# Kernel optimization log

Hardware: AMD Instinct MI355X
Metric: run time of the kernel (lower is better)

Reference implementation:

```python
import jax, jax.numpy as jnp
import numpy as np

B, S, D, H = 2, 2048, 1024, 16
HEAD_DIM = D // H
SCALE = HEAD_DIM ** -0.5


def setup_inputs() -> dict:
    key = jax.random.key(0)
    k1, k2, k3 = jax.random.split(key, 3)
    x = jax.random.normal(k1, (B, S, D), dtype=jnp.float32)
    # torch nn.Linear convention: weight is [out_features, in_features], y = x @ W.T + b
    W_qkv = jax.random.normal(k2, (3 * D, D), dtype=jnp.float32) * 0.02  # qkv Linear, bias=False
    W_out = jax.random.normal(k3, (D, D), dtype=jnp.float32) * 0.02
    b_out = jnp.zeros((D,), dtype=jnp.float32)
    return {"x": x, "W_qkv": W_qkv, "W_out": W_out, "b_out": b_out}


def reference(x, W_qkv, W_out, b_out):
    b, s, d_model = x.shape
    # qkv projection (no bias), then split 'b c (qkv h d) -> qkv b h c d'
    qkv = (x @ W_qkv.T).reshape(b, s, 3, H, HEAD_DIM).transpose(2, 0, 3, 1, 4)
    q, k, v = qkv[0], qkv[1], qkv[2]  # each [b, h, s, hd]
    # naive full attention: scores materialized as [b, h, s, s]
    attn = jax.nn.softmax(jnp.einsum('bhxd,bhyd->bhxy', q, k) * SCALE, axis=-1)
    # dropout is identity (rate 0 / eval mode)
    o = jnp.einsum('bhxy,bhyd->bhxd', attn, v)
    o = o.transpose(0, 2, 1, 3).reshape(b, s, d_model)  # 'b h c d -> b c (h d)'
    return o @ W_out.T + b_out
```

## Files before the change

### kernel.cpp

```cpp
#include <hip/hip_runtime.h>


typedef __attribute__((ext_vector_type(8))) short short8;
typedef __attribute__((ext_vector_type(4))) float f32x4;
typedef unsigned short ushort_t;
typedef unsigned int uint32;

#define AS1 __attribute__((address_space(1)))
#define AS3 __attribute__((address_space(3)))

__device__ __forceinline__ void gload_lds16(const void* gp, void* lp) {
    __builtin_amdgcn_global_load_lds((const AS1 void*)gp, (AS3 void*)lp, 16, 0, 0);
}

#if __has_builtin(__builtin_amdgcn_exp2f)
#define EXP2F(x) __builtin_amdgcn_exp2f(x)
#else
#define EXP2F(x) exp2f(x)
#endif

__device__ __forceinline__ uint32 rhu(float f) { return __float_as_uint(f) + 0x8000u; }
#if __has_builtin(__builtin_amdgcn_perm)
__device__ __forceinline__ uint32 pk2bf(float a, float b) {
    return __builtin_amdgcn_perm(rhu(b), rhu(a), 0x07060302u);
}
#else
__device__ __forceinline__ uint32 pk2bf(float a, float b) {
    return (rhu(a) >> 16) | (rhu(b) & 0xffff0000u);
}
#endif
__device__ __forceinline__ ushort_t f2bf(float f) { return (ushort_t)(rhu(f) >> 16); }

__global__ void cvt_all(const float* __restrict__ x, ushort_t* __restrict__ xb,
                        const float* __restrict__ wq, ushort_t* __restrict__ wqb,
                        const float* __restrict__ wo, ushort_t* __restrict__ wob) {
    int blk = blockIdx.x;
    const float* in; ushort_t* out;
    if (blk < 4096)      { in = x;  out = xb;  }
    else if (blk < 7168) { in = wq; out = wqb; blk -= 4096; }
    else                 { in = wo; out = wob; blk -= 7168; }
    const int i = (blk * 256 + threadIdx.x) * 4;
    const float4 v = *(const float4*)(in + i);
    uint2 pk;
    pk.x = pk2bf(v.x, v.y);
    pk.y = pk2bf(v.z, v.w);
    *(uint2*)(out + i) = pk;
}

__global__ __launch_bounds__(256, 2)
void gemm_bt_bf16(const ushort_t* __restrict__ A, const ushort_t* __restrict__ B,
                  ushort_t* __restrict__ Cb, float* __restrict__ Cf,
                  const float* __restrict__ bias, ushort_t* __restrict__ vT,
                  int M, int N, int K, int ldc, float qScale) {
    __shared__ ushort_t lA[128 * 32];
    __shared__ ushort_t lB[128 * 32];
    const int tid = threadIdx.x;
    const int wave = tid >> 6, lane = tid & 63;
    const int quad = lane >> 4, l16 = lane & 15;
    const int wr = wave >> 1, wc = wave & 1;
    const int mBase = blockIdx.y * 128, nBase = blockIdx.x * 128;

    f32x4 acc[4][4];
#pragma unroll
    for (int i = 0; i < 4; i++)
#pragma unroll
        for (int j = 0; j < 4; j++) acc[i][j] = (f32x4){0.f, 0.f, 0.f, 0.f};

    const int ar = tid >> 2;
    const int ac = (((tid & 3) ^ ((ar >> 1) & 3)) * 8);
    const int rsw = ((l16 >> 1) & 3);

    const ushort_t* aptr = A + (size_t)(mBase + ar) * K + ac;
    const ushort_t* bptr = B + (size_t)(nBase + ar) * K + ac;

    for (int k0 = 0; k0 < K; k0 += 32) {
#pragma unroll
        for (int c = 0; c < 2; c++) {
            gload_lds16(aptr + (size_t)(c * 64) * K + k0, lA + c * 2048 + wave * 512);
            gload_lds16(bptr + (size_t)(c * 64) * K + k0, lB + c * 2048 + wave * 512);
        }
        __syncthreads();

        short8 af[4], bf[4];
#pragma unroll
        for (int i = 0; i < 4; i++)
            af[i] = *(const short8*)(lA + (wr * 64 + i * 16 + l16) * 32 + ((quad ^ rsw) * 8));
#pragma unroll
        for (int j = 0; j < 4; j++)
            bf[j] = *(const short8*)(lB + (wc * 64 + j * 16 + l16) * 32 + ((quad ^ rsw) * 8));
#pragma unroll
        for (int i = 0; i < 4; i++)
#pragma unroll
            for (int j = 0; j < 4; j++)
                acc[i][j] = __builtin_amdgcn_mfma_f32_16x16x32_bf16(af[i], bf[j], acc[i][j], 0, 0, 0);
        __syncthreads();
    }

    if (vT && nBase >= 2048) {
#pragma unroll
        for (int i = 0; i < 4; i++)
#pragma unroll
            for (int j = 0; j < 4; j++) {
                const int row0 = mBase + wr * 64 + i * 16 + quad * 4;
                const int col = nBase + wc * 64 + j * 16 + l16 - 2048;
                const int b = row0 >> 11, s0 = row0 & 2047;
                uint2 pk;
                pk.x = pk2bf(acc[i][j][0], acc[i][j][1]);
                pk.y = pk2bf(acc[i][j][2], acc[i][j][3]);
                *(uint2*)(vT + ((size_t)(b * 16) * 64 + col) * 2048 + s0) = pk;
            }
        return;
    }
    const float cs = (vT && nBase < 1024) ? qScale : 1.0f;
#pragma unroll
    for (int i = 0; i < 4; i++)
#pragma unroll
        for (int j = 0; j < 4; j++)
#pragma unroll
            for (int r = 0; r < 4; r++) {
                const int row = mBase + wr * 64 + i * 16 + quad * 4 + r;
                const int col = nBase + wc * 64 + j * 16 + l16;
                const float v = acc[i][j][r];
                if (Cb) Cb[(size_t)row * ldc + col] = f2bf(v * cs);
                else    Cf[(size_t)row * ldc + col] = v + bias[col];
            }
}

__global__ __launch_bounds__(256, 4)
void attn_flash(const ushort_t* __restrict__ qk, const ushort_t* __restrict__ vT,
                ushort_t* __restrict__ o) {
    __shared__ ushort_t lK[128 * 64];
    __shared__ ushort_t lV[64 * 128];
    __shared__ ushort_t lP[4][16 * 40];

    const int tid = threadIdx.x;
    const int wave = tid >> 6, lane = tid & 63;
    const int quad = lane >> 4, l16 = lane & 15;
    const int bh = blockIdx.y;
    const int b = bh >> 4, h = bh & 15;
    const size_t rowBase = (size_t)b * 2048;
    const int qCol = h * 64, kCol = 1024 + h * 64;
    const int qRow0 = blockIdx.x * 64;
    const int swz = (l16 & 7);

    const int sr = tid >> 3;
    const int sc = ((tid & 7) ^ (sr & 7)) * 8;
    const int vr = tid >> 4;
    const int vc = ((tid & 15) ^ (vr & 7)) * 8;

#pragma unroll
    for (int cc = 0; cc < 2; cc++)
        gload_lds16(qk + (rowBase + qRow0 + cc * 32 + sr) * 2048 + qCol + sc,
                    lK + cc * 2048 + wave * 512);
    __syncthreads();
    short8 qf[2];
#pragma unroll
    for (int ks = 0; ks < 2; ks++)
        qf[ks] = *(const short8*)(lK + (wave * 16 + l16) * 64 + (((ks * 4 + quad) ^ swz) * 8));
    __syncthreads();

    short8 onesA;
#pragma unroll
    for (int i = 0; i < 8; i++) onesA[i] = (short)0x3F80;

    f32x4 oacc[4];
    f32x4 lacc = (f32x4){0.f, 0.f, 0.f, 0.f};
#pragma unroll
    for (int dt = 0; dt < 4; dt++) oacc[dt] = (f32x4){0.f, 0.f, 0.f, 0.f};

    const ushort_t* kptr = qk + (rowBase + sr) * 2048 + kCol + sc;
    const ushort_t* vptr = vT + ((size_t)bh * 64 + vr) * 2048 + vc;

    for (int kt = 0; kt < 16; kt++) {
#pragma unroll
        for (int cc = 0; cc < 4; cc++)
            gload_lds16(kptr + (size_t)(cc * 32) * 2048, lK + cc * 2048 + wave * 512);
#pragma unroll
        for (int cc = 0; cc < 4; cc++)
            gload_lds16(vptr + (size_t)(cc * 16) * 2048, lV + cc * 2048 + wave * 512);
        kptr += 128 * 2048;
        vptr += 128;
        __syncthreads();

        f32x4 sacc[8];
#pragma unroll
        for (int mt = 0; mt < 8; mt++) {
            const short8 k0 = *(const short8*)(lK + (mt * 16 + l16) * 64 + ((quad ^ swz) * 8));
            const short8 k1 = *(const short8*)(lK + (mt * 16 + l16) * 64 + (((4 + quad) ^ swz) * 8));
            f32x4 t = (f32x4){0.f, 0.f, 0.f, 0.f};
            t = __builtin_amdgcn_mfma_f32_16x16x32_bf16(k0, qf[0], t, 0, 0, 0);
            t = __builtin_amdgcn_mfma_f32_16x16x32_bf16(k1, qf[1], t, 0, 0, 0);
            sacc[mt] = t;
        }

#pragma unroll
        for (int kk = 0; kk < 4; kk++) {
#pragma unroll
            for (int t16 = 0; t16 < 2; t16++) {
                const f32x4 s = sacc[2 * kk + t16];
                uint2 pk;
                pk.x = pk2bf(EXP2F(s[0]), EXP2F(s[1]));
                pk.y = pk2bf(EXP2F(s[2]), EXP2F(s[3]));
                *(uint2*)(&lP[wave][l16 * 40 + t16 * 16 + quad * 4]) = pk;
            }
            const short8 pf = *(const short8*)(&lP[wave][l16 * 40 + quad * 8]);
            lacc = __builtin_amdgcn_mfma_f32_16x16x32_bf16(onesA, pf, lacc, 0, 0, 0);
#pragma unroll
            for (int dt = 0; dt < 4; dt++) {
                const short8 vf = *(const short8*)(lV + (dt * 16 + l16) * 128 +
                                                   (((kk * 4 + quad) ^ swz) * 8));
                oacc[dt] = __builtin_amdgcn_mfma_f32_16x16x32_bf16(vf, pf, oacc[dt], 0, 0, 0);
            }
        }
        __syncthreads();
    }

    const float inv = 1.0f / lacc[0];
    const size_t row = rowBase + qRow0 + wave * 16 + l16;
#pragma unroll
    for (int dt = 0; dt < 4; dt++) {
        uint2 pk;
        pk.x = pk2bf(oacc[dt][0] * inv, oacc[dt][1] * inv);
        pk.y = pk2bf(oacc[dt][2] * inv, oacc[dt][3] * inv);
        *(uint2*)(o + row * 1024 + h * 64 + dt * 16 + quad * 4) = pk;
    }
}

extern "C" void kernel_launch(void* const* d_in, const int* in_sizes, int n_in,
                              void* d_out, int out_size, void* d_ws, size_t ws_size,
                              hipStream_t stream) {
    const float* x    = (const float*)d_in[0];
    const float* Wqkv = (const float*)d_in[1];
    const float* Wout = (const float*)d_in[2];
    const float* bout = (const float*)d_in[3];
    float* out = (float*)d_out;

    ushort_t* xb    = (ushort_t*)d_ws;
    ushort_t* wqkvb = xb + (size_t)4096 * 1024;
    ushort_t* woutb = wqkvb + (size_t)3072 * 1024;
    ushort_t* qkb   = woutb + (size_t)1024 * 1024;
    ushort_t* vTb   = qkb + (size_t)4096 * 2048;
    ushort_t* ob    = xb;

    const float SC = 0.125f * 1.44269504089f;

    cvt_all<<<8192, 256, 0, stream>>>(x, xb, Wqkv, wqkvb, Wout, woutb);
    gemm_bt_bf16<<<dim3(24, 32), 256, 0, stream>>>(xb, wqkvb, qkb, nullptr, nullptr, vTb,
                                                   4096, 3072, 1024, 2048, SC);
    attn_flash<<<dim3(32, 32), 256, 0, stream>>>(qkb, vTb, ob);
    gemm_bt_bf16<<<dim3(8, 32), 256, 0, stream>>>(ob, woutb, nullptr, out, bout, nullptr,
                                                  4096, 1024, 1024, 1024, 1.0f);
}
```

Before: 199.0 us.

## Load GEMM operands straight into registers and split-K the flash attention over waves

The GEMM drops its LDS staging and has each wave read its MFMA fragments straight from global memory into registers, double-buffered in registers across k-steps. The attention kernel now runs 512 threads per block over 256 query rows. Each wave handles 64 query rows against half of each 64-key tile, K/V tiles are double-buffered in LDS, and the two key-halves are combined through LDS at the end. The goals are to remove LDS round trips and barriers in the GEMM and to get more Q reuse and overlap of loads with compute in attention. The cost is uncoalesced, redundant global reads in the GEMM, and more registers plus an extra reduction step in attention.

New measurement: 270.8 us. +36.1%, slower.

```diff
diff --git a/kernel.cpp b/kernel.cpp
--- a/kernel.cpp
+++ b/kernel.cpp
@@ -47,13 +47,11 @@
     *(uint2*)(out + i) = pk;
 }
 
-__global__ __launch_bounds__(256, 2)
-void gemm_bt_bf16(const ushort_t* __restrict__ A, const ushort_t* __restrict__ B,
-                  ushort_t* __restrict__ Cb, float* __restrict__ Cf,
-                  const float* __restrict__ bias, ushort_t* __restrict__ vT,
-                  int M, int N, int K, int ldc, float qScale) {
-    __shared__ ushort_t lA[128 * 32];
-    __shared__ ushort_t lB[128 * 32];
+__global__ __launch_bounds__(256, 3)
+void gemm_bt_direct(const ushort_t* __restrict__ A, const ushort_t* __restrict__ B,
+                    ushort_t* __restrict__ Cb, float* __restrict__ Cf,
+                    const float* __restrict__ bias, ushort_t* __restrict__ vT,
+                    int M, int N, int K, int ldc, float qScale) {
     const int tid = threadIdx.x;
     const int wave = tid >> 6, lane = tid & 63;
     const int quad = lane >> 4, l16 = lane & 15;
@@ -66,34 +64,36 @@
 #pragma unroll
         for (int j = 0; j < 4; j++) acc[i][j] = (f32x4){0.f, 0.f, 0.f, 0.f};
 
-    const int ar = tid >> 2;
-    const int ac = (((tid & 3) ^ ((ar >> 1) & 3)) * 8);
-    const int rsw = ((l16 >> 1) & 3);
-
-    const ushort_t* aptr = A + (size_t)(mBase + ar) * K + ac;
-    const ushort_t* bptr = B + (size_t)(nBase + ar) * K + ac;
-
-    for (int k0 = 0; k0 < K; k0 += 32) {
-#pragma unroll
-        for (int c = 0; c < 2; c++) {
-            gload_lds16(aptr + (size_t)(c * 64) * K + k0, lA + c * 2048 + wave * 512);
-            gload_lds16(bptr + (size_t)(c * 64) * K + k0, lB + c * 2048 + wave * 512);
-        }
-        __syncthreads();
-
-        short8 af[4], bf[4];
-#pragma unroll
-        for (int i = 0; i < 4; i++)
-            af[i] = *(const short8*)(lA + (wr * 64 + i * 16 + l16) * 32 + ((quad ^ rsw) * 8));
-#pragma unroll
-        for (int j = 0; j < 4; j++)
-            bf[j] = *(const short8*)(lB + (wc * 64 + j * 16 + l16) * 32 + ((quad ^ rsw) * 8));
-#pragma unroll
-        for (int i = 0; i < 4; i++)
-#pragma unroll
-            for (int j = 0; j < 4; j++)
-                acc[i][j] = __builtin_amdgcn_mfma_f32_16x16x32_bf16(af[i], bf[j], acc[i][j], 0, 0, 0);
-        __syncthreads();
+    const ushort_t* aP[4];
+    const ushort_t* bP[4];
+#pragma unroll
+    for (int i = 0; i < 4; i++) {
+        aP[i] = A + (size_t)(mBase + wr * 64 + i * 16 + l16) * K + quad * 8;
+        bP[i] = B + (size_t)(nBase + wc * 64 + i * 16 + l16) * K + quad * 8;
+    }
+
+    short8 a0[4], b0[4], a1[4], b1[4];
+#pragma unroll
+    for (int i = 0; i < 4; i++) { a0[i] = *(const short8*)(aP[i]); b0[i] = *(const short8*)(bP[i]); }
+
+#define G_MFMA(aa, bb)                                                                     \
+    _Pragma("unroll") for (int i = 0; i < 4; i++)                                          \
+        _Pragma("unroll") for (int j = 0; j < 4; j++)                                      \
+            acc[i][j] = __builtin_amdgcn_mfma_f32_16x16x32_bf16(aa[i], bb[j], acc[i][j], 0, 0, 0);
+
+    for (int k0 = 0; k0 < K; k0 += 64) {
+#pragma unroll
+        for (int i = 0; i < 4; i++) {
+            a1[i] = *(const short8*)(aP[i] + k0 + 32);
+            b1[i] = *(const short8*)(bP[i] + k0 + 32);
+        }
+        G_MFMA(a0, b0);
+#pragma unroll
+        for (int i = 0; i < 4; i++) {
+            a0[i] = *(const short8*)(aP[i] + k0 + 64);
+            b0[i] = *(const short8*)(bP[i] + k0 + 64);
+        }
+        G_MFMA(a1, b1);
     }
 
     if (vT && nBase >= 2048) {
@@ -120,109 +120,159 @@
             for (int r = 0; r < 4; r++) {
                 const int row = mBase + wr * 64 + i * 16 + quad * 4 + r;
                 const int col = nBase + wc * 64 + j * 16 + l16;
-                const float v = acc[i][j][r];
-                if (Cb) Cb[(size_t)row * ldc + col] = f2bf(v * cs);
-                else    Cf[(size_t)row * ldc + col] = v + bias[col];
-            }
-}
-
-__global__ __launch_bounds__(256, 4)
+                if (Cb) Cb[(size_t)row * ldc + col] = f2bf(acc[i][j][r] * cs);
+                else    Cf[(size_t)row * ldc + col] = acc[i][j][r] + bias[col];
+            }
+}
+
+__global__ __launch_bounds__(512, 2)
 void attn_flash(const ushort_t* __restrict__ qk, const ushort_t* __restrict__ vT,
                 ushort_t* __restrict__ o) {
-    __shared__ ushort_t lK[128 * 64];
-    __shared__ ushort_t lV[64 * 128];
-    __shared__ ushort_t lP[4][16 * 40];
+    __shared__ ushort_t smem[32768];
 
     const int tid = threadIdx.x;
     const int wave = tid >> 6, lane = tid & 63;
     const int quad = lane >> 4, l16 = lane & 15;
-    const int bh = blockIdx.y;
-    const int b = bh >> 4, h = bh & 15;
+    const int qg = wave & 3, kg = wave >> 2;
+    const int bh = blockIdx.y, b = bh >> 4, h = bh & 15;
     const size_t rowBase = (size_t)b * 2048;
     const int qCol = h * 64, kCol = 1024 + h * 64;
-    const int qRow0 = blockIdx.x * 64;
-    const int swz = (l16 & 7);
-
-    const int sr = tid >> 3;
-    const int sc = ((tid & 7) ^ (sr & 7)) * 8;
-    const int vr = tid >> 4;
-    const int vc = ((tid & 15) ^ (vr & 7)) * 8;
-
-#pragma unroll
-    for (int cc = 0; cc < 2; cc++)
-        gload_lds16(qk + (rowBase + qRow0 + cc * 32 + sr) * 2048 + qCol + sc,
-                    lK + cc * 2048 + wave * 512);
-    __syncthreads();
-    short8 qf[2];
-#pragma unroll
-    for (int ks = 0; ks < 2; ks++)
-        qf[ks] = *(const short8*)(lK + (wave * 16 + l16) * 64 + (((ks * 4 + quad) ^ swz) * 8));
+    const int qRow0 = blockIdx.x * 256;
+    const int swz = l16 & 7;
+
+    ushort_t* lP = smem + 16384 + wave * 2048;
+
+    {
+        const int rl = wave * 8 + (lane >> 3);
+#pragma unroll
+        for (int cc = 0; cc < 4; cc++) {
+            const int qr = cc * 64 + rl;
+            gload_lds16(qk + (rowBase + qRow0 + qr) * 2048 + qCol + (((lane & 7) ^ (qr & 7)) * 8),
+                        smem + 16384 + (cc * 8 + wave) * 512);
+        }
+    }
+    __syncthreads();
+    short8 qf[4][2];
+#pragma unroll
+    for (int qt = 0; qt < 4; qt++)
+#pragma unroll
+        for (int ks = 0; ks < 2; ks++)
+            qf[qt][ks] = *(const short8*)(smem + 16384 + (qg * 64 + qt * 16 + l16) * 64 +
+                                          (((ks * 4 + quad) ^ swz) * 8));
     __syncthreads();
 
     short8 onesA;
 #pragma unroll
     for (int i = 0; i < 8; i++) onesA[i] = (short)0x3F80;
 
-    f32x4 oacc[4];
-    f32x4 lacc = (f32x4){0.f, 0.f, 0.f, 0.f};
-#pragma unroll
-    for (int dt = 0; dt < 4; dt++) oacc[dt] = (f32x4){0.f, 0.f, 0.f, 0.f};
-
-    const ushort_t* kptr = qk + (rowBase + sr) * 2048 + kCol + sc;
-    const ushort_t* vptr = vT + ((size_t)bh * 64 + vr) * 2048 + vc;
-
-    for (int kt = 0; kt < 16; kt++) {
-#pragma unroll
-        for (int cc = 0; cc < 4; cc++)
-            gload_lds16(kptr + (size_t)(cc * 32) * 2048, lK + cc * 2048 + wave * 512);
-#pragma unroll
-        for (int cc = 0; cc < 4; cc++)
-            gload_lds16(vptr + (size_t)(cc * 16) * 2048, lV + cc * 2048 + wave * 512);
-        kptr += 128 * 2048;
-        vptr += 128;
+    f32x4 oacc[4][4];
+    f32x4 lacc[4];
+#pragma unroll
+    for (int dt = 0; dt < 4; dt++) {
+        lacc[dt] = (f32x4){0.f, 0.f, 0.f, 0.f};
+#pragma unroll
+        for (int qt = 0; qt < 4; qt++) oacc[dt][qt] = (f32x4){0.f, 0.f, 0.f, 0.f};
+    }
+
+    const int sr = wave * 8 + (lane >> 3);
+    const int sch = ((lane & 7) ^ (sr & 7)) * 8;
+    const ushort_t* kptr = qk + (rowBase + sr) * 2048 + kCol + sch;
+    const ushort_t* vptr = vT + ((size_t)bh * 64 + sr) * 2048 + sch;
+
+#define AT_STAGE(buf, kt)                                                            \
+    {                                                                                \
+        gload_lds16(kptr + (size_t)(kt) * 64 * 2048, smem + (buf) * 4096 + wave * 512); \
+        gload_lds16(vptr + (kt) * 64, smem + 8192 + (buf) * 4096 + wave * 512);      \
+    }
+
+    AT_STAGE(0, 0);
+    for (int kt = 0; kt < 32; kt++) {
+        const int cur = kt & 1;
         __syncthreads();
-
-        f32x4 sacc[8];
-#pragma unroll
-        for (int mt = 0; mt < 8; mt++) {
-            const short8 k0 = *(const short8*)(lK + (mt * 16 + l16) * 64 + ((quad ^ swz) * 8));
-            const short8 k1 = *(const short8*)(lK + (mt * 16 + l16) * 64 + (((4 + quad) ^ swz) * 8));
-            f32x4 t = (f32x4){0.f, 0.f, 0.f, 0.f};
-            t = __builtin_amdgcn_mfma_f32_16x16x32_bf16(k0, qf[0], t, 0, 0, 0);
-            t = __builtin_amdgcn_mfma_f32_16x16x32_bf16(k1, qf[1], t, 0, 0, 0);
-            sacc[mt] = t;
-        }
-
-#pragma unroll
-        for (int kk = 0; kk < 4; kk++) {
-#pragma unroll
-            for (int t16 = 0; t16 < 2; t16++) {
-                const f32x4 s = sacc[2 * kk + t16];
+        if (kt < 31) AT_STAGE(cur ^ 1, kt + 1);
+        const ushort_t* lK = smem + cur * 4096;
+        const ushort_t* lV = smem + 8192 + cur * 4096;
+
+        f32x4 sacc[2][4];
+#pragma unroll
+        for (int mh = 0; mh < 2; mh++) {
+            const int krow = kg * 32 + mh * 16 + l16;
+            const short8 k0 = *(const short8*)(lK + krow * 64 + ((quad ^ swz) * 8));
+            const short8 k1 = *(const short8*)(lK + krow * 64 + (((4 + quad) ^ swz) * 8));
+#pragma unroll
+            for (int qt = 0; qt < 4; qt++) {
+                f32x4 t = (f32x4){0.f, 0.f, 0.f, 0.f};
+                t = __builtin_amdgcn_mfma_f32_16x16x32_bf16(k0, qf[qt][0], t, 0, 0, 0);
+                t = __builtin_amdgcn_mfma_f32_16x16x32_bf16(k1, qf[qt][1], t, 0, 0, 0);
+                sacc[mh][qt] = t;
+            }
+        }
+
+#pragma unroll
+        for (int qt = 0; qt < 4; qt++)
+#pragma unroll
+            for (int mh = 0; mh < 2; mh++) {
+                const f32x4 s = sacc[mh][qt];
                 uint2 pk;
                 pk.x = pk2bf(EXP2F(s[0]), EXP2F(s[1]));
                 pk.y = pk2bf(EXP2F(s[2]), EXP2F(s[3]));
-                *(uint2*)(&lP[wave][l16 * 40 + t16 * 16 + quad * 4]) = pk;
-            }
-            const short8 pf = *(const short8*)(&lP[wave][l16 * 40 + quad * 8]);
-            lacc = __builtin_amdgcn_mfma_f32_16x16x32_bf16(onesA, pf, lacc, 0, 0, 0);
+                *(uint2*)(lP + (qt * 16 + l16) * 32 +
+                          (((mh * 2 + (quad >> 1)) ^ (l16 & 3)) * 8 + (quad & 1) * 4)) = pk;
+            }
+
+        short8 pf[4];
+#pragma unroll
+        for (int qt = 0; qt < 4; qt++) {
+            pf[qt] = *(const short8*)(lP + (qt * 16 + l16) * 32 + ((quad ^ (l16 & 3)) * 8));
+            lacc[qt] = __builtin_amdgcn_mfma_f32_16x16x32_bf16(onesA, pf[qt], lacc[qt], 0, 0, 0);
+        }
+#pragma unroll
+        for (int dt = 0; dt < 4; dt++) {
+            const short8 vf = *(const short8*)(lV + (dt * 16 + l16) * 64 +
+                                               (((kg * 4 + quad) ^ swz) * 8));
+#pragma unroll
+            for (int qt = 0; qt < 4; qt++)
+                oacc[dt][qt] = __builtin_amdgcn_mfma_f32_16x16x32_bf16(vf, pf[qt], oacc[dt][qt], 0, 0, 0);
+        }
+    }
+
+    float* red = (float*)smem;
+    __syncthreads();
+    if (kg == 1) {
+#pragma unroll
+        for (int qt = 0; qt < 4; qt++) red[(qg * 4 + qt) * 64 + lane] = lacc[qt][0];
+    }
+    __syncthreads();
+    float linv[4];
+    if (kg == 0) {
+#pragma unroll
+        for (int qt = 0; qt < 4; qt++)
+            linv[qt] = 1.0f / (lacc[qt][0] + red[(qg * 4 + qt) * 64 + lane]);
+    }
+    __syncthreads();
+    if (kg == 1) {
+#pragma unroll
+        for (int dt = 0; dt < 4; dt++)
+#pragma unroll
+            for (int qt = 0; qt < 4; qt++)
+                *(f32x4*)(red + (((qg * 4 + dt) * 4 + qt) * 64 + lane) * 4) = oacc[dt][qt];
+    }
+    __syncthreads();
+    if (kg == 0) {
+#pragma unroll
+        for (int qt = 0; qt < 4; qt++) {
+            const size_t row = rowBase + qRow0 + qg * 64 + qt * 16 + l16;
 #pragma unroll
             for (int dt = 0; dt < 4; dt++) {
-                const short8 vf = *(const short8*)(lV + (dt * 16 + l16) * 128 +
-                                                   (((kk * 4 + quad) ^ swz) * 8));
-                oacc[dt] = __builtin_amdgcn_mfma_f32_16x16x32_bf16(vf, pf, oacc[dt], 0, 0, 0);
-            }
-        }
-        __syncthreads();
-    }
-
-    const float inv = 1.0f / lacc[0];
-    const size_t row = rowBase + qRow0 + wave * 16 + l16;
-#pragma unroll
-    for (int dt = 0; dt < 4; dt++) {
-        uint2 pk;
-        pk.x = pk2bf(oacc[dt][0] * inv, oacc[dt][1] * inv);
-        pk.y = pk2bf(oacc[dt][2] * inv, oacc[dt][3] * inv);
-        *(uint2*)(o + row * 1024 + h * 64 + dt * 16 + quad * 4) = pk;
+                const f32x4 r = *(const f32x4*)(red + (((qg * 4 + dt) * 4 + qt) * 64 + lane) * 4);
+                uint2 pk;
+                pk.x = pk2bf((oacc[dt][qt][0] + r[0]) * linv[qt],
+                             (oacc[dt][qt][1] + r[1]) * linv[qt]);
+                pk.y = pk2bf((oacc[dt][qt][2] + r[2]) * linv[qt],
+                             (oacc[dt][qt][3] + r[3]) * linv[qt]);
+                *(uint2*)(o + row * 1024 + h * 64 + dt * 16 + quad * 4) = pk;
+            }
+        }
     }
 }
 
@@ -245,9 +295,9 @@
     const float SC = 0.125f * 1.44269504089f;
 
     cvt_all<<<8192, 256, 0, stream>>>(x, xb, Wqkv, wqkvb, Wout, woutb);
-    gemm_bt_bf16<<<dim3(24, 32), 256, 0, stream>>>(xb, wqkvb, qkb, nullptr, nullptr, vTb,
-                                                   4096, 3072, 1024, 2048, SC);
-    attn_flash<<<dim3(32, 32), 256, 0, stream>>>(qkb, vTb, ob);
-    gemm_bt_bf16<<<dim3(8, 32), 256, 0, stream>>>(ob, woutb, nullptr, out, bout, nullptr,
-                                                  4096, 1024, 1024, 1024, 1.0f);
-}
+    gemm_bt_direct<<<dim3(24, 32), 256, 0, stream>>>(xb, wqkvb, qkb, nullptr, nullptr, vTb,
+                                                     4096, 3072, 1024, 2048, SC);
+    attn_flash<<<dim3(8, 32), 512, 0, stream>>>(qkb, vTb, ob);
+    gemm_bt_direct<<<dim3(8, 32), 256, 0, stream>>>(ob, woutb, nullptr, out, bout, nullptr,
+                                                    4096, 1024, 1024, 1024, 1.0f);
+}
```
